# Performance work log

Hardware: AMD Instinct MI355X
Metric: run time of the kernel (lower is better)

The kernel has to match this reference:

```python
import jax, jax.numpy as jnp
import numpy as np

N = 50000
E = 600000
D_IN = 128
D_OUT = 128
EPS = 1e-12  # F.normalize eps


def setup_inputs() -> dict:
    key = jax.random.key(0)
    ks = jax.random.split(key, 10)
    s = 1.0 / np.sqrt(D_IN)
    inp = {
        "x": jax.random.normal(ks[0], (N, D_IN), dtype=jnp.float32),
        "edge_index": jax.random.randint(ks[1], (2, E), 0, N, dtype=jnp.int64),
        # conv1: lin_l (with bias) applied to aggregated neighbors, lin_r (no bias) to root
        "W1l": jax.random.uniform(ks[2], (D_IN, D_IN), jnp.float32, -s, s),
        "b1": jax.random.uniform(ks[3], (D_IN,), jnp.float32, -s, s),
        "W1r": jax.random.uniform(ks[4], (D_IN, D_IN), jnp.float32, -s, s),
        # conv2
        "W2l": jax.random.uniform(ks[5], (D_IN, D_OUT), jnp.float32, -s, s),
        "b2": jax.random.uniform(ks[6], (D_OUT,), jnp.float32, -s, s),
        "W2r": jax.random.uniform(ks[7], (D_IN, D_OUT), jnp.float32, -s, s),
        # final fc
        "Wf": jax.random.uniform(ks[8], (D_OUT, D_OUT), jnp.float32, -s, s),
        "bf": jax.random.uniform(ks[9], (D_OUT,), jnp.float32, -s, s),
    }
    return inp


def _sage_conv(x, src, dst, Wl, bl, Wr):
    # mean-aggregate messages from source nodes onto destination nodes
    msgs = x[src]  # [E, d] gather
    agg = jax.ops.segment_sum(msgs, dst, num_segments=N)  # [N, d]
    cnt = jax.ops.segment_sum(jnp.ones((src.shape[0],), x.dtype), dst, num_segments=N)
    agg = agg / jnp.maximum(cnt, 1.0)[:, None]  # isolated nodes -> 0
    out = agg @ Wl + bl + x @ Wr
    # L2 normalize per node (PyG normalize=True)
    nrm = jnp.sqrt(jnp.sum(out * out, axis=-1, keepdims=True))
    return out / jnp.maximum(nrm, EPS)


def reference(x, edge_index, W1l, b1, W1r, W2l, b2, W2r, Wf, bf):
    src, dst = edge_index[0], edge_index[1]
    h = jax.nn.relu(_sage_conv(x, src, dst, W1l, b1, W1r))
    h = jax.nn.relu(_sage_conv(h, src, dst, W2l, b2, W2r))
    return h @ Wf + bf
```

## Files before the change

kernel.cpp:

```cpp
#include <hip/hip_runtime.h>
#include <hip/hip_fp16.h>

#define D 128
#define SCAN_B 256
#define HLD 136

typedef __attribute__((ext_vector_type(8))) short bf16x8;
typedef __attribute__((ext_vector_type(4))) float f32x4;

__device__ __forceinline__ unsigned short f2bf(float f) {
    unsigned u = __float_as_uint(f);
    unsigned r = u + 0x7FFFu + ((u >> 16) & 1u);
    return (unsigned short)(r >> 16);
}
__device__ __forceinline__ float bf2f(unsigned short h) {
    return __uint_as_float(((unsigned)h) << 16);
}

__global__ void count_kernel(const int* __restrict__ ei, int E, int* __restrict__ cnt) {
    int t = blockIdx.x * blockDim.x + threadIdx.x;
    if (t < E) atomicAdd(&cnt[ei[E + t]], 1);
}

__global__ void scan_pass1(const int* __restrict__ cnt, int* __restrict__ rs,
                           int* __restrict__ bsum, int N) {
    __shared__ int lds[SCAN_B];
    int tid = threadIdx.x;
    int i = blockIdx.x * SCAN_B + tid;
    int v = (i < N) ? cnt[i] : 0;
    lds[tid] = v;
    __syncthreads();
    for (int o = 1; o < SCAN_B; o <<= 1) {
        int t = (tid >= o) ? lds[tid - o] : 0;
        __syncthreads();
        lds[tid] += t;
        __syncthreads();
    }
    if (i < N) rs[i] = lds[tid] - v;
    if (tid == SCAN_B - 1) bsum[blockIdx.x] = lds[tid];
}

__global__ void scan_pass2(int* __restrict__ bsum, int nb) {
    __shared__ int lds[SCAN_B];
    int tid = threadIdx.x;
    int v = (tid < nb) ? bsum[tid] : 0;
    lds[tid] = v;
    __syncthreads();
    for (int o = 1; o < SCAN_B; o <<= 1) {
        int t = (tid >= o) ? lds[tid - o] : 0;
        __syncthreads();
        lds[tid] += t;
        __syncthreads();
    }
    if (tid < nb) bsum[tid] = lds[tid] - v;
}

__global__ void scan_pass3(int* __restrict__ rs, int* __restrict__ cursor,
                           const int* __restrict__ bsum, const int* __restrict__ cnt,
                           float* __restrict__ inv, int N) {
    int i = blockIdx.x * SCAN_B + threadIdx.x;
    if (i < N) {
        int v = rs[i] + bsum[blockIdx.x];
        rs[i] = v;
        cursor[i] = v;
        inv[i] = 1.0f / (float)max(cnt[i], 1);
    }
}

__global__ void fill_kernel(const int* __restrict__ ei, int E,
                            int* __restrict__ cursor, int* __restrict__ csr) {
    int e = blockIdx.x * blockDim.x + threadIdx.x;
    if (e < E) {
        int src = ei[e], dst = ei[E + e];
        int pos = atomicAdd(&cursor[dst], 1);
        csr[pos] = src;
    }
}

__global__ void cvt_half_kernel(const float* __restrict__ x, __half* __restrict__ xh, int n8) {
    int i = blockIdx.x * blockDim.x + threadIdx.x;
    if (i >= n8) return;
    const float4* x4 = (const float4*)x;
    float4 a = x4[2 * i], b = x4[2 * i + 1];
    __half2 h0 = __floats2half2_rn(a.x, a.y);
    __half2 h1 = __floats2half2_rn(a.z, a.w);
    __half2 h2 = __floats2half2_rn(b.x, b.y);
    __half2 h3 = __floats2half2_rn(b.z, b.w);
    uint4 o;
    o.x = *(const unsigned*)&h0;
    o.y = *(const unsigned*)&h1;
    o.z = *(const unsigned*)&h2;
    o.w = *(const unsigned*)&h3;
    ((uint4*)xh)[i] = o;
}

__device__ __forceinline__ void acc8(uint4 v, float* s) {
    const __half2* h = reinterpret_cast<const __half2*>(&v);
    float2 f0 = __half22float2(h[0]);
    float2 f1 = __half22float2(h[1]);
    float2 f2 = __half22float2(h[2]);
    float2 f3 = __half22float2(h[3]);
    s[0] += f0.x; s[1] += f0.y; s[2] += f1.x; s[3] += f1.y;
    s[4] += f2.x; s[5] += f2.y; s[6] += f3.x; s[7] += f3.y;
}

__global__ void aggregate_kernel(const __half* __restrict__ xh, const int* __restrict__ csr,
                                 const int* __restrict__ rs, const int* __restrict__ cnt,
                                 const float* __restrict__ inv, float* __restrict__ agg,
                                 int N) {
    int t = blockIdx.x * blockDim.x + threadIdx.x;
    int node = t >> 4;
    int c = t & 15;
    if (node >= N) return;
    int deg = cnt[node];
    int st = rs[node];
    const uint4* x4 = (const uint4*)xh;
    float s[8] = {0.f, 0.f, 0.f, 0.f, 0.f, 0.f, 0.f, 0.f};
    int i = 0;
    for (; i + 4 <= deg; i += 4) {
        int n0 = csr[st + i + 0], n1 = csr[st + i + 1];
        int n2 = csr[st + i + 2], n3 = csr[st + i + 3];
        uint4 v0 = x4[(size_t)n0 * 16 + c];
        uint4 v1 = x4[(size_t)n1 * 16 + c];
        uint4 v2 = x4[(size_t)n2 * 16 + c];
        uint4 v3 = x4[(size_t)n3 * 16 + c];
        acc8(v0, s); acc8(v1, s); acc8(v2, s); acc8(v3, s);
    }
    for (; i < deg; i++) {
        int n0 = csr[st + i];
        uint4 v0 = x4[(size_t)n0 * 16 + c];
        acc8(v0, s);
    }
    float iv = inv[node];
    float* dst = agg + (size_t)node * D + c * 8;
    ((float4*)dst)[0] = make_float4(s[0] * iv, s[1] * iv, s[2] * iv, s[3] * iv);
    ((float4*)dst)[1] = make_float4(s[4] * iv, s[5] * iv, s[6] * iv, s[7] * iv);
}

__global__ void pack_kernel(const float* __restrict__ W1l, const float* __restrict__ W1r,
                            const float* __restrict__ W2l, const float* __restrict__ W2r,
                            const float* __restrict__ Wf, unsigned short* __restrict__ pw) {
    int idx = blockIdx.x * blockDim.x + threadIdx.x;
    if (idx >= 5 * 2048) return;
    int w = idx >> 11;
    int r = idx & 2047;
    int ks = r >> 9;
    int t = (r >> 6) & 7;
    int lane = r & 63;
    int q = lane >> 4, n = lane & 15;
    const float* W = (w == 0) ? W1l : (w == 1) ? W1r : (w == 2) ? W2l : (w == 3) ? W2r : Wf;
    unsigned short* dh = pw + (size_t)w * 32768;
    unsigned short* dl = dh + 16384;
    int off = ((ks * 8 + t) * 64 + lane) * 8;
#pragma unroll
    for (int j = 0; j < 8; j++) {
        float v = W[(size_t)(ks * 32 + q * 8 + j) * D + t * 16 + n];
        unsigned short hb = f2bf(v);
        dh[off + j] = hb;
        dl[off + j] = f2bf(v - bf2f(hb));
    }
}

__device__ __forceinline__ void split8(const float* av, bf16x8& hi, bf16x8& lo) {
#pragma unroll
    for (int j = 0; j < 8; j++) {
        unsigned short hb = f2bf(av[j]);
        hi[j] = (short)hb;
        lo[j] = (short)f2bf(av[j] - bf2f(hb));
    }
}

template <int FUSE_FC>
__global__ __launch_bounds__(256) void mfma_gemm(
        const float* __restrict__ Aagg, const float* __restrict__ Ax,
        const unsigned short* __restrict__ W0h, const unsigned short* __restrict__ W0lo,
        const unsigned short* __restrict__ W1h, const unsigned short* __restrict__ W1lo,
        const float* __restrict__ bias,
        const unsigned short* __restrict__ Wfh, const unsigned short* __restrict__ Wflo,
        const float* __restrict__ bfin,
        float* __restrict__ out, __half* __restrict__ outh, int N) {
    __shared__ float normbuf[2][2][16];
    __shared__ unsigned short Hs[FUSE_FC ? 2 * 2 * 16 * HLD : 4];

    const int tid = threadIdx.x;
    const int lane = tid & 63;
    const int wave = tid >> 6;
    const int rg = wave >> 1;
    const int cg = wave & 1;
    const int c = lane & 15;
    const int q = lane >> 4;
    const int R = blockIdx.x * 32 + rg * 16;

    int row0 = R + c;
    if (row0 >= N) row0 = N - 1;
    const size_t a_base = (size_t)row0 * D;

    f32x4 acc[4];
#pragma unroll
    for (int t = 0; t < 4; t++)
#pragma unroll
        for (int r = 0; r < 4; r++) acc[t][r] = 0.0f;

#pragma unroll
    for (int ks = 0; ks < 8; ks++) {
        const float* Asrc = (ks < 4) ? Aagg : Ax;
        const int kl = ks & 3;
        const int koff = kl * 32 + q * 8;
        float av[8];
        *((float4*)&av[0]) = *((const float4*)(Asrc + a_base + koff));
        *((float4*)&av[4]) = *((const float4*)(Asrc + a_base + koff + 4));
        bf16x8 ah, al;
        split8(av, ah, al);

        const uint4* Wh4 = (const uint4*)((ks < 4) ? W0h : W1h);
        const uint4* Wl4 = (const uint4*)((ks < 4) ? W0lo : W1lo);
#pragma unroll
        for (int t = 0; t < 4; t++) {
            int fi = (kl * 8 + cg * 4 + t) * 64 + lane;
            bf16x8 bh = __builtin_bit_cast(bf16x8, Wh4[fi]);
            bf16x8 blo = __builtin_bit_cast(bf16x8, Wl4[fi]);
            acc[t] = __builtin_amdgcn_mfma_f32_16x16x32_bf16(ah, bh, acc[t], 0, 0, 0);
            acc[t] = __builtin_amdgcn_mfma_f32_16x16x32_bf16(al, bh, acc[t], 0, 0, 0);
            acc[t] = __builtin_amdgcn_mfma_f32_16x16x32_bf16(ah, blo, acc[t], 0, 0, 0);
        }
    }

#pragma unroll
    for (int t = 0; t < 4; t++) {
        float bv = bias[(cg * 4 + t) * 16 + c];
#pragma unroll
        for (int r = 0; r < 4; r++) acc[t][r] += bv;
    }
    float vr[4];
#pragma unroll
    for (int r = 0; r < 4; r++) {
        float v = 0.0f;
#pragma unroll
        for (int t = 0; t < 4; t++) v += acc[t][r] * acc[t][r];
        v += __shfl_xor(v, 1, 16);
        v += __shfl_xor(v, 2, 16);
        v += __shfl_xor(v, 4, 16);
        v += __shfl_xor(v, 8, 16);
        vr[r] = v;
    }
    if (c == 0) {
#pragma unroll
        for (int r = 0; r < 4; r++) normbuf[rg][cg][q * 4 + r] = vr[r];
    }
    __syncthreads();
#pragma unroll
    for (int r = 0; r < 4; r++) {
        int row = q * 4 + r;
        float tot = normbuf[rg][0][row] + normbuf[rg][1][row];
        float rn = 1.0f / fmaxf(sqrtf(tot), 1e-12f);
#pragma unroll
        for (int t = 0; t < 4; t++) acc[t][r] = fmaxf(acc[t][r] * rn, 0.0f);
    }

    if (!FUSE_FC) {
#pragma unroll
        for (int t = 0; t < 4; t++)
#pragma unroll
            for (int r = 0; r < 4; r++) {
                int row = R + q * 4 + r;
                if (row < N) {
                    float v = acc[t][r];
                    size_t idx = (size_t)row * D + (cg * 4 + t) * 16 + c;
                    out[idx] = v;
                    if (outh) outh[idx] = __float2half_rn(v);
                }
            }
        return;
    }

    unsigned short* Hhi = &Hs[rg * 2 * 16 * HLD];
    unsigned short* Hlo = Hhi + 16 * HLD;
#pragma unroll
    for (int t = 0; t < 4; t++)
#pragma unroll
        for (int r = 0; r < 4; r++) {
            int row = q * 4 + r;
            int col = (cg * 4 + t) * 16 + c;
            float hv = acc[t][r];
            unsigned short hb = f2bf(hv);
            Hhi[row * HLD + col] = hb;
            Hlo[row * HLD + col] = f2bf(hv - bf2f(hb));
        }
    __syncthreads();

    f32x4 acc2[4];
#pragma unroll
    for (int t = 0; t < 4; t++) {
        float bv = bfin[(cg * 4 + t) * 16 + c];
#pragma unroll
        for (int r = 0; r < 4; r++) acc2[t][r] = bv;
    }
    const uint4* Wfh4 = (const uint4*)Wfh;
    const uint4* Wfl4 = (const uint4*)Wflo;
#pragma unroll
    for (int ks2 = 0; ks2 < 4; ks2++) {
        bf16x8 ah2 = __builtin_bit_cast(bf16x8, *(const uint4*)&Hhi[c * HLD + ks2 * 32 + q * 8]);
        bf16x8 al2 = __builtin_bit_cast(bf16x8, *(const uint4*)&Hlo[c * HLD + ks2 * 32 + q * 8]);
#pragma unroll
        for (int t = 0; t < 4; t++) {
            int fi = (ks2 * 8 + cg * 4 + t) * 64 + lane;
            bf16x8 bh = __builtin_bit_cast(bf16x8, Wfh4[fi]);
            bf16x8 blo = __builtin_bit_cast(bf16x8, Wfl4[fi]);
            acc2[t] = __builtin_amdgcn_mfma_f32_16x16x32_bf16(ah2, bh, acc2[t], 0, 0, 0);
            acc2[t] = __builtin_amdgcn_mfma_f32_16x16x32_bf16(al2, bh, acc2[t], 0, 0, 0);
            acc2[t] = __builtin_amdgcn_mfma_f32_16x16x32_bf16(ah2, blo, acc2[t], 0, 0, 0);
        }
    }

#pragma unroll
    for (int t = 0; t < 4; t++)
#pragma unroll
        for (int r = 0; r < 4; r++) {
            int row = R + q * 4 + r;
            if (row < N) out[(size_t)row * D + (cg * 4 + t) * 16 + c] = acc2[t][r];
        }
}

extern "C" void kernel_launch(void* const* d_in, const int* in_sizes, int n_in,
                              void* d_out, int out_size, void* d_ws, size_t ws_size,
                              hipStream_t stream) {
    const float* x   = (const float*)d_in[0];
    const int*   ei  = (const int*)d_in[1];
    const float* W1l = (const float*)d_in[2];
    const float* b1  = (const float*)d_in[3];
    const float* W1r = (const float*)d_in[4];
    const float* W2l = (const float*)d_in[5];
    const float* b2  = (const float*)d_in[6];
    const float* W2r = (const float*)d_in[7];
    const float* Wf  = (const float*)d_in[8];
    const float* bf  = (const float*)d_in[9];
    float* out = (float*)d_out;

    int N = in_sizes[0] / D;
    int E = in_sizes[1] / 2;

    float* ws     = (float*)d_ws;
    float* agg    = ws;
    float* inv    = ws + (size_t)N * D;
    int*   rs     = (int*)(inv + N);
    int*   cnt    = rs + N;
    int*   cursor = cnt + N;
    int*   bsum   = cursor + N;
    int*   csr    = bsum + 256;
    unsigned short* pw = (unsigned short*)(csr + E);
    unsigned short* pW1lh = pw + 0 * 32768, *pW1ll = pW1lh + 16384;
    unsigned short* pW1rh = pw + 1 * 32768, *pW1rl = pW1rh + 16384;
    unsigned short* pW2lh = pw + 2 * 32768, *pW2ll = pW2lh + 16384;
    unsigned short* pW2rh = pw + 3 * 32768, *pW2rl = pW2rh + 16384;
    unsigned short* pWfh  = pw + 4 * 32768, *pWfl  = pWfh + 16384;
    __half* hb = (__half*)(pw + 5 * 32768);

    int nb = (N + SCAN_B - 1) / SCAN_B;

    hipMemsetAsync(cnt, 0, (size_t)N * sizeof(int), stream);
    pack_kernel<<<40, 256, 0, stream>>>(W1l, W1r, W2l, W2r, Wf, pw);
    int n8 = N * 16;
    cvt_half_kernel<<<(n8 + 255) / 256, 256, 0, stream>>>(x, hb, n8);
    count_kernel<<<(E + 255) / 256, 256, 0, stream>>>(ei, E, cnt);
    scan_pass1<<<nb, SCAN_B, 0, stream>>>(cnt, rs, bsum, N);
    scan_pass2<<<1, SCAN_B, 0, stream>>>(bsum, nb);
    scan_pass3<<<nb, SCAN_B, 0, stream>>>(rs, cursor, bsum, cnt, inv, N);
    fill_kernel<<<(E + 255) / 256, 256, 0, stream>>>(ei, E, cursor, csr);

    int agg_blocks = (N * 16 + 255) / 256;
    int gemm_blocks = (N + 31) / 32;

    aggregate_kernel<<<agg_blocks, 256, 0, stream>>>(hb, csr, rs, cnt, inv, agg, N);
    mfma_gemm<0><<<gemm_blocks, 256, 0, stream>>>(agg, x, pW1lh, pW1ll, pW1rh, pW1rl, b1,
                                                  nullptr, nullptr, nullptr, out, hb, N);

    aggregate_kernel<<<agg_blocks, 256, 0, stream>>>(hb, csr, rs, cnt, inv, agg, N);
    mfma_gemm<1><<<gemm_blocks, 256, 0, stream>>>(agg, out, pW2lh, pW2ll, pW2rh, pW2rl, b2,
                                                  pWfh, pWfl, bf, out, nullptr, N);
}
```

Before: 296.1 us.

## Switch split-precision MFMA to fp16 hi/lo, store aggregates as half pairs

Replaces the bf16 hi/lo split with an fp16 hi/lo split and uses the f16 MFMA. The aggregate kernel now writes pre-split half hi/lo buffers instead of fp32, so the GEMM no longer reconverts A operands. Layer-1 output is stored as interleaved half hi/lo rows in the output buffer, which layer 2 gathers from with a doubled stride. Each wave now computes all 128 columns for 16 rows, removing the cross-wave norm reduction and its barrier. The cost is more accumulator registers per wave and fp16 range limits on the stored values.

```diff
diff --git a/kernel.cpp b/kernel.cpp
--- a/kernel.cpp
+++ b/kernel.cpp
@@ -5,17 +5,8 @@
 #define SCAN_B 256
 #define HLD 136
 
-typedef __attribute__((ext_vector_type(8))) short bf16x8;
+typedef __attribute__((ext_vector_type(8))) _Float16 f16x8;
 typedef __attribute__((ext_vector_type(4))) float f32x4;
-
-__device__ __forceinline__ unsigned short f2bf(float f) {
-    unsigned u = __float_as_uint(f);
-    unsigned r = u + 0x7FFFu + ((u >> 16) & 1u);
-    return (unsigned short)(r >> 16);
-}
-__device__ __forceinline__ float bf2f(unsigned short h) {
-    return __uint_as_float(((unsigned)h) << 16);
-}
 
 __global__ void count_kernel(const int* __restrict__ ei, int E, int* __restrict__ cnt) {
     int t = blockIdx.x * blockDim.x + threadIdx.x;
@@ -104,10 +95,11 @@
     s[4] += f2.x; s[5] += f2.y; s[6] += f3.x; s[7] += f3.y;
 }
 
-__global__ void aggregate_kernel(const __half* __restrict__ xh, const int* __restrict__ csr,
+__global__ void aggregate_kernel(const __half* __restrict__ xh, int sstride,
+                                 const int* __restrict__ csr,
                                  const int* __restrict__ rs, const int* __restrict__ cnt,
-                                 const float* __restrict__ inv, float* __restrict__ agg,
-                                 int N) {
+                                 const float* __restrict__ inv,
+                                 __half* __restrict__ aggh, __half* __restrict__ aggl, int N) {
     int t = blockIdx.x * blockDim.x + threadIdx.x;
     int node = t >> 4;
     int c = t & 15;
@@ -120,21 +112,31 @@
     for (; i + 4 <= deg; i += 4) {
         int n0 = csr[st + i + 0], n1 = csr[st + i + 1];
         int n2 = csr[st + i + 2], n3 = csr[st + i + 3];
-        uint4 v0 = x4[(size_t)n0 * 16 + c];
-        uint4 v1 = x4[(size_t)n1 * 16 + c];
-        uint4 v2 = x4[(size_t)n2 * 16 + c];
-        uint4 v3 = x4[(size_t)n3 * 16 + c];
+        uint4 v0 = x4[(size_t)n0 * sstride + c];
+        uint4 v1 = x4[(size_t)n1 * sstride + c];
+        uint4 v2 = x4[(size_t)n2 * sstride + c];
+        uint4 v3 = x4[(size_t)n3 * sstride + c];
         acc8(v0, s); acc8(v1, s); acc8(v2, s); acc8(v3, s);
     }
     for (; i < deg; i++) {
         int n0 = csr[st + i];
-        uint4 v0 = x4[(size_t)n0 * 16 + c];
+        uint4 v0 = x4[(size_t)n0 * sstride + c];
         acc8(v0, s);
     }
     float iv = inv[node];
-    float* dst = agg + (size_t)node * D + c * 8;
-    ((float4*)dst)[0] = make_float4(s[0] * iv, s[1] * iv, s[2] * iv, s[3] * iv);
-    ((float4*)dst)[1] = make_float4(s[4] * iv, s[5] * iv, s[6] * iv, s[7] * iv);
+    uint4 oh, ol;
+    __half2* ph = (__half2*)&oh;
+    __half2* pl = (__half2*)&ol;
+#pragma unroll
+    for (int jj = 0; jj < 4; jj++) {
+        float v0 = s[2 * jj] * iv, v1 = s[2 * jj + 1] * iv;
+        __half h0 = __float2half_rn(v0), h1 = __float2half_rn(v1);
+        ph[jj] = __halves2half2(h0, h1);
+        pl[jj] = __halves2half2(__float2half_rn(v0 - __half2float(h0)),
+                                __float2half_rn(v1 - __half2float(h1)));
+    }
+    ((uint4*)aggh)[(size_t)node * 16 + c] = oh;
+    ((uint4*)aggl)[(size_t)node * 16 + c] = ol;
 }
 
 __global__ void pack_kernel(const float* __restrict__ W1l, const float* __restrict__ W1r,
@@ -155,169 +157,187 @@
 #pragma unroll
     for (int j = 0; j < 8; j++) {
         float v = W[(size_t)(ks * 32 + q * 8 + j) * D + t * 16 + n];
-        unsigned short hb = f2bf(v);
-        dh[off + j] = hb;
-        dl[off + j] = f2bf(v - bf2f(hb));
-    }
-}
-
-__device__ __forceinline__ void split8(const float* av, bf16x8& hi, bf16x8& lo) {
-#pragma unroll
-    for (int j = 0; j < 8; j++) {
-        unsigned short hb = f2bf(av[j]);
-        hi[j] = (short)hb;
-        lo[j] = (short)f2bf(av[j] - bf2f(hb));
-    }
-}
-
-template <int FUSE_FC>
+        __half hb = __float2half_rn(v);
+        dh[off + j] = __half_as_ushort(hb);
+        dl[off + j] = __half_as_ushort(__float2half_rn(v - __half2float(hb)));
+    }
+}
+
+__device__ __forceinline__ void split_f16(const float* v, uint4& hi, uint4& lo) {
+    __half2* ph = (__half2*)&hi;
+    __half2* pl = (__half2*)&lo;
+#pragma unroll
+    for (int jj = 0; jj < 4; jj++) {
+        __half h0 = __float2half_rn(v[2 * jj]);
+        __half h1 = __float2half_rn(v[2 * jj + 1]);
+        ph[jj] = __halves2half2(h0, h1);
+        pl[jj] = __halves2half2(__float2half_rn(v[2 * jj] - __half2float(h0)),
+                                __float2half_rn(v[2 * jj + 1] - __half2float(h1)));
+    }
+}
+
+template <int LAYER>
 __global__ __launch_bounds__(256) void mfma_gemm(
-        const float* __restrict__ Aagg, const float* __restrict__ Ax,
-        const unsigned short* __restrict__ W0h, const unsigned short* __restrict__ W0lo,
-        const unsigned short* __restrict__ W1h, const unsigned short* __restrict__ W1lo,
+        const uint4* __restrict__ Agh, const uint4* __restrict__ Agl,
+        const float* __restrict__ Xf,
+        const uint4* Hio,
+        const uint4* __restrict__ W0h, const uint4* __restrict__ W0l,
+        const uint4* __restrict__ W1h, const uint4* __restrict__ W1l,
         const float* __restrict__ bias,
-        const unsigned short* __restrict__ Wfh, const unsigned short* __restrict__ Wflo,
-        const float* __restrict__ bfin,
-        float* __restrict__ out, __half* __restrict__ outh, int N) {
-    __shared__ float normbuf[2][2][16];
-    __shared__ unsigned short Hs[FUSE_FC ? 2 * 2 * 16 * HLD : 4];
+        const uint4* __restrict__ W2h, const uint4* __restrict__ W2l,
+        const float* __restrict__ bias2,
+        float* out, __half* Hout, int N) {
+    __shared__ __half Hs[(LAYER == 2) ? 4 * 2 * 16 * HLD : 4];
 
     const int tid = threadIdx.x;
     const int lane = tid & 63;
     const int wave = tid >> 6;
-    const int rg = wave >> 1;
-    const int cg = wave & 1;
     const int c = lane & 15;
     const int q = lane >> 4;
-    const int R = blockIdx.x * 32 + rg * 16;
-
+    const int R = blockIdx.x * 64 + wave * 16;
     int row0 = R + c;
     if (row0 >= N) row0 = N - 1;
-    const size_t a_base = (size_t)row0 * D;
-
-    f32x4 acc[4];
-#pragma unroll
-    for (int t = 0; t < 4; t++)
+
+    uint4 Ah_[8], Al_[8];
+    const size_t rb16 = (size_t)row0 * 16 + q;
+#pragma unroll
+    for (int kl = 0; kl < 4; kl++) {
+        Ah_[kl] = Agh[rb16 + kl * 4];
+        Al_[kl] = Agl[rb16 + kl * 4];
+    }
+    if (LAYER == 1) {
+        const float4* xf4 = (const float4*)Xf;
+        const size_t xb = (size_t)row0 * 32 + q * 2;
+        float4 xa[8];
+#pragma unroll
+        for (int kl = 0; kl < 4; kl++) {
+            xa[2 * kl] = xf4[xb + kl * 8];
+            xa[2 * kl + 1] = xf4[xb + kl * 8 + 1];
+        }
+#pragma unroll
+        for (int kl = 0; kl < 4; kl++) {
+            float v[8] = {xa[2 * kl].x, xa[2 * kl].y, xa[2 * kl].z, xa[2 * kl].w,
+                          xa[2 * kl + 1].x, xa[2 * kl + 1].y, xa[2 * kl + 1].z, xa[2 * kl + 1].w};
+            split_f16(v, Ah_[4 + kl], Al_[4 + kl]);
+        }
+    } else {
+        const size_t rb32 = (size_t)row0 * 32 + q;
+#pragma unroll
+        for (int kl = 0; kl < 4; kl++) {
+            Ah_[4 + kl] = Hio[rb32 + kl * 4];
+            Al_[4 + kl] = Hio[rb32 + 16 + kl * 4];
+        }
+    }
+
+    f32x4 acc[8];
+#pragma unroll
+    for (int t = 0; t < 8; t++)
 #pragma unroll
         for (int r = 0; r < 4; r++) acc[t][r] = 0.0f;
 
 #pragma unroll
     for (int ks = 0; ks < 8; ks++) {
-        const float* Asrc = (ks < 4) ? Aagg : Ax;
-        const int kl = ks & 3;
-        const int koff = kl * 32 + q * 8;
-        float av[8];
-        *((float4*)&av[0]) = *((const float4*)(Asrc + a_base + koff));
-        *((float4*)&av[4]) = *((const float4*)(Asrc + a_base + koff + 4));
-        bf16x8 ah, al;
-        split8(av, ah, al);
-
-        const uint4* Wh4 = (const uint4*)((ks < 4) ? W0h : W1h);
-        const uint4* Wl4 = (const uint4*)((ks < 4) ? W0lo : W1lo);
-#pragma unroll
-        for (int t = 0; t < 4; t++) {
-            int fi = (kl * 8 + cg * 4 + t) * 64 + lane;
-            bf16x8 bh = __builtin_bit_cast(bf16x8, Wh4[fi]);
-            bf16x8 blo = __builtin_bit_cast(bf16x8, Wl4[fi]);
-            acc[t] = __builtin_amdgcn_mfma_f32_16x16x32_bf16(ah, bh, acc[t], 0, 0, 0);
-            acc[t] = __builtin_amdgcn_mfma_f32_16x16x32_bf16(al, bh, acc[t], 0, 0, 0);
-            acc[t] = __builtin_amdgcn_mfma_f32_16x16x32_bf16(ah, blo, acc[t], 0, 0, 0);
-        }
-    }
-
-#pragma unroll
-    for (int t = 0; t < 4; t++) {
-        float bv = bias[(cg * 4 + t) * 16 + c];
+        const uint4* Wh = ((ks < 4) ? W0h : W1h) + (size_t)(ks & 3) * 512 + lane;
+        const uint4* Wl = ((ks < 4) ? W0l : W1l) + (size_t)(ks & 3) * 512 + lane;
+        f16x8 ah = __builtin_bit_cast(f16x8, Ah_[ks]);
+        f16x8 al = __builtin_bit_cast(f16x8, Al_[ks]);
+#pragma unroll
+        for (int t = 0; t < 8; t++) {
+            f16x8 bh = __builtin_bit_cast(f16x8, Wh[t * 64]);
+            f16x8 bl = __builtin_bit_cast(f16x8, Wl[t * 64]);
+            acc[t] = __builtin_amdgcn_mfma_f32_16x16x32_f16(ah, bh, acc[t], 0, 0, 0);
+            acc[t] = __builtin_amdgcn_mfma_f32_16x16x32_f16(al, bh, acc[t], 0, 0, 0);
+            acc[t] = __builtin_amdgcn_mfma_f32_16x16x32_f16(ah, bl, acc[t], 0, 0, 0);
+        }
+    }
+
+#pragma unroll
+    for (int t = 0; t < 8; t++) {
+        float bv = bias[t * 16 + c];
 #pragma unroll
         for (int r = 0; r < 4; r++) acc[t][r] += bv;
     }
-    float vr[4];
 #pragma unroll
     for (int r = 0; r < 4; r++) {
         float v = 0.0f;
 #pragma unroll
-        for (int t = 0; t < 4; t++) v += acc[t][r] * acc[t][r];
+        for (int t = 0; t < 8; t++) v += acc[t][r] * acc[t][r];
         v += __shfl_xor(v, 1, 16);
         v += __shfl_xor(v, 2, 16);
         v += __shfl_xor(v, 4, 16);
         v += __shfl_xor(v, 8, 16);
-        vr[r] = v;
-    }
-    if (c == 0) {
-#pragma unroll
-        for (int r = 0; r < 4; r++) normbuf[rg][cg][q * 4 + r] = vr[r];
-    }
-    __syncthreads();
-#pragma unroll
-    for (int r = 0; r < 4; r++) {
-        int row = q * 4 + r;
-        float tot = normbuf[rg][0][row] + normbuf[rg][1][row];
-        float rn = 1.0f / fmaxf(sqrtf(tot), 1e-12f);
-#pragma unroll
-        for (int t = 0; t < 4; t++) acc[t][r] = fmaxf(acc[t][r] * rn, 0.0f);
-    }
-
-    if (!FUSE_FC) {
-#pragma unroll
-        for (int t = 0; t < 4; t++)
+        float rn = 1.0f / fmaxf(sqrtf(v), 1e-12f);
+#pragma unroll
+        for (int t = 0; t < 8; t++) acc[t][r] = fmaxf(acc[t][r] * rn, 0.0f);
+    }
+
+    if (LAYER == 1) {
+#pragma unroll
+        for (int t = 0; t < 8; t++)
 #pragma unroll
             for (int r = 0; r < 4; r++) {
                 int row = R + q * 4 + r;
                 if (row < N) {
                     float v = acc[t][r];
-                    size_t idx = (size_t)row * D + (cg * 4 + t) * 16 + c;
-                    out[idx] = v;
-                    if (outh) outh[idx] = __float2half_rn(v);
+                    __half h = __float2half_rn(v);
+                    size_t base = (size_t)row * 256;
+                    Hout[base + t * 16 + c] = h;
+                    Hout[base + 128 + t * 16 + c] = __float2half_rn(v - __half2float(h));
                 }
             }
         return;
     }
 
-    unsigned short* Hhi = &Hs[rg * 2 * 16 * HLD];
-    unsigned short* Hlo = Hhi + 16 * HLD;
-#pragma unroll
-    for (int t = 0; t < 4; t++)
+    __half* hh = &Hs[wave * (2 * 16 * HLD)];
+    __half* hl = hh + 16 * HLD;
+#pragma unroll
+    for (int t = 0; t < 8; t++)
 #pragma unroll
         for (int r = 0; r < 4; r++) {
-            int row = q * 4 + r;
-            int col = (cg * 4 + t) * 16 + c;
-            float hv = acc[t][r];
-            unsigned short hb = f2bf(hv);
-            Hhi[row * HLD + col] = hb;
-            Hlo[row * HLD + col] = f2bf(hv - bf2f(hb));
+            int m = q * 4 + r;
+            float v = acc[t][r];
+            __half h = __float2half_rn(v);
+            hh[m * HLD + t * 16 + c] = h;
+            hl[m * HLD + t * 16 + c] = __float2half_rn(v - __half2float(h));
         }
     __syncthreads();
 
-    f32x4 acc2[4];
-#pragma unroll
-    for (int t = 0; t < 4; t++) {
-        float bv = bfin[(cg * 4 + t) * 16 + c];
+    uint4 a2h_[4], a2l_[4];
+#pragma unroll
+    for (int k2 = 0; k2 < 4; k2++) {
+        a2h_[k2] = *(const uint4*)&hh[c * HLD + k2 * 32 + q * 8];
+        a2l_[k2] = *(const uint4*)&hl[c * HLD + k2 * 32 + q * 8];
+    }
+
+    f32x4 acc2[8];
+#pragma unroll
+    for (int t = 0; t < 8; t++) {
+        float bv = bias2[t * 16 + c];
 #pragma unroll
         for (int r = 0; r < 4; r++) acc2[t][r] = bv;
     }
-    const uint4* Wfh4 = (const uint4*)Wfh;
-    const uint4* Wfl4 = (const uint4*)Wflo;
-#pragma unroll
-    for (int ks2 = 0; ks2 < 4; ks2++) {
-        bf16x8 ah2 = __builtin_bit_cast(bf16x8, *(const uint4*)&Hhi[c * HLD + ks2 * 32 + q * 8]);
-        bf16x8 al2 = __builtin_bit_cast(bf16x8, *(const uint4*)&Hlo[c * HLD + ks2 * 32 + q * 8]);
-#pragma unroll
-        for (int t = 0; t < 4; t++) {
-            int fi = (ks2 * 8 + cg * 4 + t) * 64 + lane;
-            bf16x8 bh = __builtin_bit_cast(bf16x8, Wfh4[fi]);
-            bf16x8 blo = __builtin_bit_cast(bf16x8, Wfl4[fi]);
-            acc2[t] = __builtin_amdgcn_mfma_f32_16x16x32_bf16(ah2, bh, acc2[t], 0, 0, 0);
-            acc2[t] = __builtin_amdgcn_mfma_f32_16x16x32_bf16(al2, bh, acc2[t], 0, 0, 0);
-            acc2[t] = __builtin_amdgcn_mfma_f32_16x16x32_bf16(ah2, blo, acc2[t], 0, 0, 0);
-        }
-    }
-
-#pragma unroll
-    for (int t = 0; t < 4; t++)
+#pragma unroll
+    for (int k2 = 0; k2 < 4; k2++) {
+        const uint4* Wh = W2h + (size_t)k2 * 512 + lane;
+        const uint4* Wl = W2l + (size_t)k2 * 512 + lane;
+        f16x8 ah = __builtin_bit_cast(f16x8, a2h_[k2]);
+        f16x8 al = __builtin_bit_cast(f16x8, a2l_[k2]);
+#pragma unroll
+        for (int t = 0; t < 8; t++) {
+            f16x8 bh = __builtin_bit_cast(f16x8, Wh[t * 64]);
+            f16x8 bl = __builtin_bit_cast(f16x8, Wl[t * 64]);
+            acc2[t] = __builtin_amdgcn_mfma_f32_16x16x32_f16(ah, bh, acc2[t], 0, 0, 0);
+            acc2[t] = __builtin_amdgcn_mfma_f32_16x16x32_f16(al, bh, acc2[t], 0, 0, 0);
+            acc2[t] = __builtin_amdgcn_mfma_f32_16x16x32_f16(ah, bl, acc2[t], 0, 0, 0);
+        }
+    }
+
+#pragma unroll
+    for (int t = 0; t < 8; t++)
 #pragma unroll
         for (int r = 0; r < 4; r++) {
             int row = R + q * 4 + r;
-            if (row < N) out[(size_t)row * D + (cg * 4 + t) * 16 + c] = acc2[t][r];
+            if (row < N) out[(size_t)row * D + t * 16 + c] = acc2[t][r];
         }
 }
 
@@ -339,28 +359,30 @@
     int N = in_sizes[0] / D;
     int E = in_sizes[1] / 2;
 
-    float* ws     = (float*)d_ws;
-    float* agg    = ws;
-    float* inv    = ws + (size_t)N * D;
+    __half* Agh = (__half*)d_ws;
+    __half* Agl = Agh + (size_t)N * D;
+    __half* Xh  = Agl + (size_t)N * D;
+    float* inv  = (float*)(Xh + (size_t)N * D);
     int*   rs     = (int*)(inv + N);
     int*   cnt    = rs + N;
     int*   cursor = cnt + N;
     int*   bsum   = cursor + N;
     int*   csr    = bsum + 256;
     unsigned short* pw = (unsigned short*)(csr + E);
-    unsigned short* pW1lh = pw + 0 * 32768, *pW1ll = pW1lh + 16384;
-    unsigned short* pW1rh = pw + 1 * 32768, *pW1rl = pW1rh + 16384;
-    unsigned short* pW2lh = pw + 2 * 32768, *pW2ll = pW2lh + 16384;
-    unsigned short* pW2rh = pw + 3 * 32768, *pW2rl = pW2rh + 16384;
-    unsigned short* pWfh  = pw + 4 * 32768, *pWfl  = pWfh + 16384;
-    __half* hb = (__half*)(pw + 5 * 32768);
+    unsigned short* p1lh = pw + 0 * 32768, *p1ll = p1lh + 16384;
+    unsigned short* p1rh = pw + 1 * 32768, *p1rl = p1rh + 16384;
+    unsigned short* p2lh = pw + 2 * 32768, *p2ll = p2lh + 16384;
+    unsigned short* p2rh = pw + 3 * 32768, *p2rl = p2rh + 16384;
+    unsigned short* pfh  = pw + 4 * 32768, *pfl  = pfh + 16384;
+
+    __half* H1 = (__half*)d_out;
 
     int nb = (N + SCAN_B - 1) / SCAN_B;
 
     hipMemsetAsync(cnt, 0, (size_t)N * sizeof(int), stream);
     pack_kernel<<<40, 256, 0, stream>>>(W1l, W1r, W2l, W2r, Wf, pw);
     int n8 = N * 16;
-    cvt_half_kernel<<<(n8 + 255) / 256, 256, 0, stream>>>(x, hb, n8);
+    cvt_half_kernel<<<(n8 + 255) / 256, 256, 0, stream>>>(x, Xh, n8);
     count_kernel<<<(E + 255) / 256, 256, 0, stream>>>(ei, E, cnt);
     scan_pass1<<<nb, SCAN_B, 0, stream>>>(cnt, rs, bsum, N);
     scan_pass2<<<1, SCAN_B, 0, stream>>>(bsum, nb);
@@ -368,13 +390,17 @@
     fill_kernel<<<(E + 255) / 256, 256, 0, stream>>>(ei, E, cursor, csr);
 
     int agg_blocks = (N * 16 + 255) / 256;
-    int gemm_blocks = (N + 31) / 32;
-
-    aggregate_kernel<<<agg_blocks, 256, 0, stream>>>(hb, csr, rs, cnt, inv, agg, N);
-    mfma_gemm<0><<<gemm_blocks, 256, 0, stream>>>(agg, x, pW1lh, pW1ll, pW1rh, pW1rl, b1,
-                                                  nullptr, nullptr, nullptr, out, hb, N);
-
-    aggregate_kernel<<<agg_blocks, 256, 0, stream>>>(hb, csr, rs, cnt, inv, agg, N);
-    mfma_gemm<1><<<gemm_blocks, 256, 0, stream>>>(agg, out, pW2lh, pW2ll, pW2rh, pW2rl, b2,
-                                                  pWfh, pWfl, bf, out, nullptr, N);
-}
+    int gemm_blocks = (N + 63) / 64;
+
+    aggregate_kernel<<<agg_blocks, 256, 0, stream>>>(Xh, 16, csr, rs, cnt, inv, Agh, Agl, N);
+    mfma_gemm<1><<<gemm_blocks, 256, 0, stream>>>(
+        (const uint4*)Agh, (const uint4*)Agl, x, nullptr,
+        (const uint4*)p1lh, (const uint4*)p1ll, (const uint4*)p1rh, (const uint4*)p1rl, b1,
+        nullptr, nullptr, nullptr, nullptr, H1, N);
+
+    aggregate_kernel<<<agg_blocks, 256, 0, stream>>>(H1, 32, csr, rs, cnt, inv, Agh, Agl, N);
+    mfma_gemm<2><<<gemm_blocks, 256, 0, stream>>>(
+        (const uint4*)Agh, (const uint4*)Agl, nullptr, (const uint4*)d_out,
+        (const uint4*)p2lh, (const uint4*)p2ll, (const uint4*)p2rh, (const uint4*)p2rl, b2,
+        (const uint4*)pfh, (const uint4*)pfl, bf, out, nullptr, N);
+}
```

Result: faster. 280.5 us (-5.3%).
